# Kernel optimization log

Measured on AMD Instinct MI355X. Metric: run time of the kernel, lower is better.

The kernel has to match this reference:

```python
import jax, jax.numpy as jnp
import numpy as np
from jax import lax

B, G = 8, 64
V = G * G * G  # 262144, matches fc1 in-features


def setup_inputs() -> dict:
    key = jax.random.key(0)
    ks = jax.random.split(key, 10)
    boundary = (jax.random.uniform(ks[0], (B, 1, G, G, G)) < 0.1).astype(jnp.float32)
    conv1_w = jax.random.normal(ks[1], (64, 1, 3, 3, 3), jnp.float32) * 0.1
    conv1_b = jax.random.normal(ks[2], (64,), jnp.float32) * 0.01
    conv2_w = jax.random.normal(ks[3], (1, 64, 3, 3, 3), jnp.float32) * 0.05
    conv2_b = jax.random.normal(ks[4], (1,), jnp.float32) * 0.01
    fc1_w = jax.random.normal(ks[5], (256, V), jnp.float32) * (1.0 / np.sqrt(V))
    fc1_b = jax.random.normal(ks[6], (256,), jnp.float32) * 0.01
    fc2_w = jax.random.normal(ks[7], (1, 256), jnp.float32) * (1.0 / 16.0)
    fc2_b = jax.random.normal(ks[8], (1,), jnp.float32) * 0.01
    noise = jax.random.uniform(ks[9], (B, V), jnp.float32)
    return {"boundary": boundary, "conv1_w": conv1_w, "conv1_b": conv1_b,
            "conv2_w": conv2_w, "conv2_b": conv2_b, "fc1_w": fc1_w,
            "fc1_b": fc1_b, "fc2_w": fc2_w, "fc2_b": fc2_b,
            "noise": noise, "num_points": 10}


def _conv3d(x, w, b):
    # NCDHW / OIDHW, stride 1, padding 1 with k=3 -> SAME
    y = lax.conv_general_dilated(x, w, (1, 1, 1), 'SAME',
                                 dimension_numbers=('NCDHW', 'OIDHW', 'NCDHW'))
    return y + b[None, :, None, None, None]


def _generate_points(boundary, noise, num_points):
    # Vectorized equivalent of the per-point rejection loop:
    # uniform sampling without replacement over cells where boundary == 0.
    bflat = boundary.reshape(boundary.shape[0], -1)  # [B, V]
    scores = jnp.where(bflat > 0.5, -jnp.inf, noise)
    _, idx = lax.top_k(scores, num_points)  # [B, k]
    rows = jnp.arange(bflat.shape[0])[:, None]
    pts = jnp.zeros_like(bflat).at[rows, idx].set(1.0)
    return pts.reshape(boundary.shape)


def reference(boundary, conv1_w, conv1_b, conv2_w, conv2_b,
              fc1_w, fc1_b, fc2_w, fc2_b, noise, num_points):
    x = jax.nn.relu(_conv3d(boundary, conv1_w, conv1_b))
    x = jax.nn.relu(_conv3d(x, conv2_w, conv2_b))
    x = x.reshape(x.shape[0], -1)                      # [B, V]
    x = jax.nn.relu(x @ fc1_w.T + fc1_b)               # [B, 256]
    probability = jax.nn.sigmoid(x @ fc2_w.T + fc2_b) * 100.0  # [B, 1]
    points = _generate_points(boundary, noise, num_points)
    return points, probability
```

## Files before the change

### kernel.cpp

```cpp
#include <hip/hip_runtime.h>
#include <math.h>

#define G 64
#define GV (G*G*G)
#define NB 8
#define NP 9

typedef unsigned short u16;
typedef unsigned int u32;
typedef unsigned long long U64;
typedef __bf16 bf16x8 __attribute__((ext_vector_type(8)));
typedef float f32x4 __attribute__((ext_vector_type(4)));

union BF8 { u16 s[8]; bf16x8 v; };

__device__ __forceinline__ float bf2f(u16 h) {
    union { u32 u; float f; } c; c.u = ((u32)h) << 16; return c.f;
}
__device__ __forceinline__ u16 f2bf(float f) {
    union { float f; u32 u; } c; c.f = f;
    u32 u = c.u;
    return (u16)((u + 0x7fffu + ((u >> 16) & 1u)) >> 16);
}
__device__ __forceinline__ u32 cvt_pk_bf16(float lo, float hi) {
    u32 r;
    asm volatile("v_cvt_pk_bf16_f32 %0, %1, %2" : "=v"(r) : "v"(lo), "v"(hi));
    return r;
}

#define YSTRIDE 36

__global__ __launch_bounds__(256) void convA_mfma_kernel(
    const float* __restrict__ bnd,
    const float* __restrict__ w1, const float* __restrict__ b1,
    const float* __restrict__ w2,
    u16* __restrict__ zbuf)
{
    int b = blockIdx.y;
    const float* bd = bnd + (size_t)b * GV;
    u16* zb = zbuf + (size_t)b * (NP * (size_t)GV);

    __shared__ __align__(16) u16 halo[2378];
    __shared__ __align__(16) u32 Ylds[4][66 * YSTRIDE];

    int tid = threadIdx.x;
    int z0 = (blockIdx.x >> 4) * 4, y0 = (blockIdx.x & 15) * 4;

    {
        float* ldsW = (float*)&Ylds[0][0];
        for (int i = tid; i < 3520; i += 256) {
            float v;
            if (i < 1728)      v = w1[i];
            else if (i < 3456) v = w2[i - 1728];
            else               v = b1[i - 3456];
            ldsW[i] = v;
        }
    }

    for (int i = tid; i < 2378; i += 256) {
        u16 hval = 0;
        if (i < 2376) {
            int hz = i / 396, rem = i - hz * 396;
            int hy = rem / 66, hx = rem - hy * 66;
            int gz = z0 + hz - 1, gy = y0 + hy - 1, gx = hx - 1;
            if (((unsigned)gz < (unsigned)G) & ((unsigned)gy < (unsigned)G) &
                ((unsigned)gx < (unsigned)G)) {
                float f = bd[(gz << 12) + (gy << 6) + gx];
                hval = (f > 0.5f) ? (u16)0x3F80 : (u16)0;
            }
        }
        halo[i] = hval;
    }

    __syncthreads();

    int wv = tid >> 6, lane = tid & 63;
    int g = lane >> 4, lr = lane & 15;

    const float* ldsW = (const float*)&Ylds[0][0];
    BF8 w1A[4];
#pragma unroll
    for (int m = 0; m < 4; m++) {
        int c = 16 * m + lr;
#pragma unroll
        for (int j = 0; j < 8; j++) {
            int kk = 8 * g + j;
            float w = (kk < 27) ? ldsW[c * 27 + kk] : 0.0f;
            w1A[m].s[j] = f2bf(w);
        }
    }
    BF8 w2dx[3][2];
#pragma unroll
    for (int dx = 0; dx < 3; dx++)
#pragma unroll
        for (int ks = 0; ks < 2; ks++)
#pragma unroll
            for (int j = 0; j < 8; j++) {
                int ch = 32 * ks + 8 * g + j;
                float w = (lr < NP) ? ldsW[1728 + ch * 27 + 3 * lr + dx] : 0.0f;
                w2dx[dx][ks].s[j] = f2bf(w);
            }
    float bias[4][4];
#pragma unroll
    for (int m = 0; m < 4; m++)
#pragma unroll
        for (int r = 0; r < 4; r++) bias[m][r] = ldsW[3456 + 16 * m + 4 * g + r];

    int tapoff[8];
#pragma unroll
    for (int j = 0; j < 8; j++) {
        int kk = 8 * g + j;
        int kc = kk < 27 ? kk : 0;
        int dz = kc / 9, ry = kc - dz * 9;
        int dy = ry / 3, dxx = ry - dy * 3;
        tapoff[j] = dz * 396 + dy * 66 + dxx;
    }

    __syncthreads();

    u32* myY = &Ylds[wv][0];

    for (int li = 0; li < 4; li++) {
        int l = wv * 4 + li;
        int zl = l >> 2, yl = l & 3;
        int linebase = (zl * 6 + yl) * 66 + lr;
        int vbase = ((z0 + zl) << 12) + ((y0 + yl) << 6);

        myY[(lane < 32 ? 0 : 65 * YSTRIDE) + (lane & 31)] = 0;

        for (int xt = 0; xt < 4; xt++) {
            int x0 = xt * 16;
            BF8 xB;
#pragma unroll
            for (int j = 0; j < 8; j++)
                xB.s[j] = halo[linebase + x0 + tapoff[j]];

            f32x4 yac[4];
#pragma unroll
            for (int m = 0; m < 4; m++) {
                f32x4 c0;
                c0[0] = bias[m][0]; c0[1] = bias[m][1];
                c0[2] = bias[m][2]; c0[3] = bias[m][3];
                yac[m] = __builtin_amdgcn_mfma_f32_16x16x32_bf16(
                    w1A[m].v, xB.v, c0, 0, 0, 0);
            }

            int rx = x0 + lr + 1;
#pragma unroll
            for (int m = 0; m < 4; m++) {
                float a0 = fmaxf(yac[m][0], 0.f), a1 = fmaxf(yac[m][1], 0.f);
                float a2 = fmaxf(yac[m][2], 0.f), a3 = fmaxf(yac[m][3], 0.f);
                u32 h01 = cvt_pk_bf16(a0, a1);
                u32 h23 = cvt_pk_bf16(a2, a3);
                *(U64*)&myY[rx * YSTRIDE + 8 * m + 2 * g] =
                    (U64)h01 | ((U64)h23 << 32);
            }
        }

        asm volatile("" ::: "memory");

        for (int xt = 0; xt < 4; xt++) {
            int x0 = xt * 16;
            f32x4 zac = f32x4{0.f, 0.f, 0.f, 0.f};
#pragma unroll
            for (int dx = 0; dx < 3; dx++) {
                int rbase = (x0 + lr + dx) * YSTRIDE;
#pragma unroll
                for (int ks = 0; ks < 2; ks++) {
                    bf16x8 yB = *(const bf16x8*)&myY[rbase + 16 * ks + 4 * g];
                    zac = __builtin_amdgcn_mfma_f32_16x16x32_bf16(
                        w2dx[dx][ks].v, yB, zac, 0, 0, 0);
                }
            }

            int vg = vbase + x0 + lr;
#pragma unroll
            for (int r = 0; r < 4; r++) {
                int p = 4 * g + r;
                if (p < NP)
                    zb[(size_t)p * GV + vg] = f2bf(zac[r]);
            }
        }

        asm volatile("" ::: "memory");
    }
}

#define BPB 32
#define IDXM 0x3FFFFu

__global__ __launch_bounds__(256) void convB_topk_kernel(
    const u16* __restrict__ zbuf, float* __restrict__ xout,
    const float* __restrict__ b2,
    const float* __restrict__ bnd, const float* __restrict__ noise,
    U64* __restrict__ cand, float4* __restrict__ pts_out)
{
    __shared__ U64 lcand[256 * 10];
    __shared__ U64 rv[256];
    __shared__ int rp[256];

    int tid = threadIdx.x;

    if (blockIdx.x >= 256) {
        int r = blockIdx.x - 256;
        int vblk = r & 1023, b = r >> 10;
        const u16* zb = zbuf + (size_t)b * (NP * (size_t)GV);
        float* xo = xout + (size_t)b * GV;

        int v  = vblk * 256 + tid;
        int zc = v >> 12, yc = (v >> 6) & 63, xc = v & 63;
        float acc = b2[0];
#pragma unroll
        for (int dz = 0; dz < 3; dz++)
#pragma unroll
        for (int dy = 0; dy < 3; dy++) {
            int p = dz * 3 + dy;
            int zz = zc + dz - 1, yy = yc + dy - 1;
            bool ok = ((unsigned)zz < (unsigned)G) & ((unsigned)yy < (unsigned)G);
            if (ok) acc += bf2f(zb[(size_t)p * GV + (zz << 12) + (yy << 6) + xc]);
        }
        xo[v] = fmaxf(acc, 0.0f);
        return;
    }

    int blk = blockIdx.x & 31;
    int b   = blockIdx.x >> 5;
    int vbase = blk * (GV / BPB);

    float4* zp = pts_out + ((size_t)b * GV + vbase) / 4;
#pragma unroll
    for (int i = 0; i < 8; i++)
        zp[i * 256 + tid] = make_float4(0.f, 0.f, 0.f, 0.f);

    const float* bd = bnd + (size_t)b * GV + vbase;
    const float* nz = noise + (size_t)b * GV + vbase;

    U64 top[10];
#pragma unroll
    for (int k = 0; k < 10; k++) top[k] = 0ull;

    for (int i = 0; i < (GV / BPB) / 256; i++) {
        int e = i * 256 + tid;
        float bv = bd[e];
        float s  = nz[e];
        U64 p = (bv > 0.5f) ? 0ull
              : ((((U64)__float_as_uint(s)) << 32) |
                 (IDXM - (unsigned)(vbase + e)));
        if (p > top[9]) {
#pragma unroll
            for (int k = 0; k < 10; k++) {
                U64 mx = p > top[k] ? p : top[k];
                U64 mn = p > top[k] ? top[k] : p;
                top[k] = mx; p = mn;
            }
        }
    }

#pragma unroll
    for (int k = 0; k < 10; k++) lcand[tid * 10 + k] = top[k];
    __syncthreads();

    for (int pass = 0; pass < 10; pass++) {
        U64 bv = 0; int bp = 0;
        for (int i = tid; i < 2560; i += 256) {
            U64 xv = lcand[i];
            if (xv > bv) { bv = xv; bp = i; }
        }
        rv[tid] = bv; rp[tid] = bp;
        __syncthreads();
        for (int off = 128; off > 0; off >>= 1) {
            if (tid < off) {
                if (rv[tid + off] > rv[tid]) { rv[tid] = rv[tid + off]; rp[tid] = rp[tid + off]; }
            }
            __syncthreads();
        }
        if (tid == 0) {
            cand[((size_t)b * BPB + blk) * 10 + pass] = rv[0];
            lcand[rp[0]] = 0ull;
        }
        __syncthreads();
    }
}

__global__ __launch_bounds__(256) void fc1_kernel(
    const float* __restrict__ W, const float* __restrict__ x,
    float* __restrict__ pacc)
{
    int bid = blockIdx.x;
    int xcd  = bid & 7;
    int slot = bid >> 3;
    int vc = (xcd << 3) | (slot >> 5);
    int jt = slot & 31;
    int tid = threadIdx.x;
    int j0 = jt * 8;
    size_t v0 = (size_t)vc * 4096;

    const f32x4* Wp[8];
#pragma unroll
    for (int jj = 0; jj < 8; jj++)
        Wp[jj] = reinterpret_cast<const f32x4*>(W + (size_t)(j0 + jj) * GV + v0);
    const f32x4* Xp[NB];
#pragma unroll
    for (int b = 0; b < NB; b++)
        Xp[b] = reinterpret_cast<const f32x4*>(x + (size_t)b * GV + v0);

    float acc[8][NB];
#pragma unroll
    for (int jj = 0; jj < 8; jj++)
#pragma unroll
        for (int b = 0; b < NB; b++) acc[jj][b] = 0.0f;

    for (int i = 0; i < 4; i++) {
        int e = i * 256 + tid;
        f32x4 wvv[8];
#pragma unroll
        for (int jj = 0; jj < 8; jj++)
            wvv[jj] = __builtin_nontemporal_load(&Wp[jj][e]);
        f32x4 xv[NB];
#pragma unroll
        for (int b = 0; b < NB; b++) xv[b] = Xp[b][e];
#pragma unroll
        for (int b = 0; b < NB; b++) {
#pragma unroll
            for (int jj = 0; jj < 8; jj++) {
                acc[jj][b] = fmaf(wvv[jj][0], xv[b][0], acc[jj][b]);
                acc[jj][b] = fmaf(wvv[jj][1], xv[b][1], acc[jj][b]);
                acc[jj][b] = fmaf(wvv[jj][2], xv[b][2], acc[jj][b]);
                acc[jj][b] = fmaf(wvv[jj][3], xv[b][3], acc[jj][b]);
            }
        }
    }

    __shared__ float sacc[256][36];
    __shared__ float p2[8][40];
#pragma unroll
    for (int pass = 0; pass < 2; pass++) {
        if (pass > 0) __syncthreads();
        float4* row = reinterpret_cast<float4*>(&sacc[tid][0]);
#pragma unroll
        for (int jj = 0; jj < 4; jj++) {
            int js = pass * 4 + jj;
            row[jj * 2 + 0] = make_float4(acc[js][0], acc[js][1], acc[js][2], acc[js][3]);
            row[jj * 2 + 1] = make_float4(acc[js][4], acc[js][5], acc[js][6], acc[js][7]);
        }
        __syncthreads();
        {
            int o = tid & 31, gg = tid >> 5;
            float s = 0.0f;
#pragma unroll
            for (int k = 0; k < 32; k++) s += sacc[gg * 32 + k][o];
            p2[gg][o] = s;
        }
        __syncthreads();
        if (tid < 32) {
            float s = 0.0f;
#pragma unroll
            for (int gg = 0; gg < 8; gg++) s += p2[gg][tid];
            int jj = tid >> 3, b = tid & 7;
            pacc[((size_t)b * 64 + vc) * 256 + (j0 + pass * 4 + jj)] = s;
        }
    }
}

__global__ __launch_bounds__(256) void finalize_kernel(
    const U64* __restrict__ cand, float* __restrict__ pts,
    const float* __restrict__ pacc, const float* __restrict__ fc1_b,
    const float* __restrict__ fc2_w, const float* __restrict__ fc2_b,
    float* __restrict__ prob)
{
    int tid = threadIdx.x;

    if (blockIdx.x < 8) {
        int b = blockIdx.x;
        __shared__ U64 lc[BPB * 10];
        __shared__ U64 rv[256];
        __shared__ int rp[256];
        __shared__ int widx[10];
        for (int i = tid; i < BPB * 10; i += 256) lc[i] = cand[(size_t)b * BPB * 10 + i];
        __syncthreads();

        for (int pass = 0; pass < 10; pass++) {
            U64 bv = 0; int bp = 0;
            for (int i = tid; i < BPB * 10; i += 256) {
                U64 xv = lc[i];
                if (xv > bv) { bv = xv; bp = i; }
            }
            rv[tid] = bv; rp[tid] = bp;
            __syncthreads();
            for (int off = 128; off > 0; off >>= 1) {
                if (tid < off) {
                    if (rv[tid + off] > rv[tid]) { rv[tid] = rv[tid + off]; rp[tid] = rp[tid + off]; }
                }
                __syncthreads();
            }
            if (tid == 0) { widx[pass] = (int)(IDXM - (u32)(rv[0] & 0xffffffffu)); lc[rp[0]] = 0ull; }
            __syncthreads();
        }
        if (tid < 10) pts[(size_t)b * GV + widx[tid]] = 1.0f;
    } else {
        int j = tid;
        float h[NB];
#pragma unroll
        for (int b = 0; b < NB; b++) h[b] = 0.0f;
        for (int c = 0; c < 64; c++) {
#pragma unroll
            for (int b = 0; b < NB; b++)
                h[b] += pacc[((size_t)b * 64 + c) * 256 + j];
        }
        float w2j = fc2_w[j];
        float contrib[NB];
#pragma unroll
        for (int b = 0; b < NB; b++)
            contrib[b] = fmaxf(h[b] + fc1_b[j], 0.0f) * w2j;

        int lane = j & 63, wid = j >> 6;
#pragma unroll
        for (int b = 0; b < NB; b++)
#pragma unroll
            for (int off = 32; off > 0; off >>= 1)
                contrib[b] += __shfl_down(contrib[b], off, 64);

        __shared__ float sred[4][NB];
        if (lane == 0) {
#pragma unroll
            for (int b = 0; b < NB; b++) sred[wid][b] = contrib[b];
        }
        __syncthreads();
        if (j < NB) {
            float t = sred[0][j] + sred[1][j] + sred[2][j] + sred[3][j] + fc2_b[0];
            prob[j] = 100.0f / (1.0f + expf(-t));
        }
    }
}

extern "C" void kernel_launch(void* const* d_in, const int* in_sizes, int n_in,
                              void* d_out, int out_size, void* d_ws, size_t ws_size,
                              hipStream_t stream)
{
    const float* bnd   = (const float*)d_in[0];
    const float* w1    = (const float*)d_in[1];
    const float* b1    = (const float*)d_in[2];
    const float* w2    = (const float*)d_in[3];
    const float* b2    = (const float*)d_in[4];
    const float* fw1   = (const float*)d_in[5];
    const float* fb1   = (const float*)d_in[6];
    const float* fw2   = (const float*)d_in[7];
    const float* fb2   = (const float*)d_in[8];
    const float* noise = (const float*)d_in[9];

    float* out = (float*)d_out;
    char* ws = (char*)d_ws;

    const size_t xbuf_off = 0;
    const size_t pacc_off = xbuf_off + (size_t)NB * GV * 4;
    const size_t cand_off = pacc_off + (size_t)NB * 64 * 256 * 4;
    const size_t zbuf_off = cand_off + (size_t)NB * BPB * 10 * 8;

    float* xbuf = (float*)(ws + xbuf_off);
    float* pacc = (float*)(ws + pacc_off);
    U64*   cand = (U64*)(ws + cand_off);
    u16*   zbuf = (u16*)(ws + zbuf_off);

    dim3 gA(256, NB);
    convA_mfma_kernel<<<gA, 256, 0, stream>>>(bnd, w1, b1, w2, zbuf);

    convB_topk_kernel<<<8448, 256, 0, stream>>>(zbuf, xbuf, b2, bnd, noise,
                                                cand, (float4*)out);

    fc1_kernel<<<2048, 256, 0, stream>>>(fw1, xbuf, pacc);

    finalize_kernel<<<9, 256, 0, stream>>>(cand, out, pacc, fb1, fw2, fb2,
                                           out + (size_t)NB * GV);
}
```

Before: 172.2 us.

## Move top-k point sampling from convB launch into convA launch

The top-k candidate selection and point-zeroing blocks move out of the convB kernel and into the convA kernel as extra leading blocks. Their shared memory is overlaid with convA's halo and Y buffers in one pool. The aim is to run the memory-bound top-k work alongside the compute-bound MFMA conv, so the convB launch only does the cheap stencil sum. The cost is a larger shared-memory footprint per block, which may lower convA occupancy, and top-k blocks may finish unevenly relative to the conv blocks.

```diff
diff --git a/kernel.cpp b/kernel.cpp
--- a/kernel.cpp
+++ b/kernel.cpp
@@ -29,25 +29,97 @@
 }
 
 #define YSTRIDE 36
-
-__global__ __launch_bounds__(256) void convA_mfma_kernel(
+#define BPB 32
+#define IDXM 0x3FFFFu
+#define POOLB 42784
+
+__global__ __launch_bounds__(256) void convA_topk_kernel(
     const float* __restrict__ bnd,
     const float* __restrict__ w1, const float* __restrict__ b1,
     const float* __restrict__ w2,
-    u16* __restrict__ zbuf)
+    u16* __restrict__ zbuf,
+    const float* __restrict__ noise,
+    U64* __restrict__ cand, float4* __restrict__ pts_out)
 {
-    int b = blockIdx.y;
+    __shared__ __align__(16) char pool[POOLB];
+    int tid = threadIdx.x;
+
+    if (blockIdx.x < 256) {
+        int blk = blockIdx.x & 31;
+        int b   = blockIdx.x >> 5;
+        int vbase = blk * (GV / BPB);
+
+        float4* zp = pts_out + ((size_t)b * GV + vbase) / 4;
+#pragma unroll
+        for (int i = 0; i < 8; i++)
+            zp[i * 256 + tid] = make_float4(0.f, 0.f, 0.f, 0.f);
+
+        const float* bd = bnd + (size_t)b * GV + vbase;
+        const float* nz = noise + (size_t)b * GV + vbase;
+
+        U64 top[10];
+#pragma unroll
+        for (int k = 0; k < 10; k++) top[k] = 0ull;
+
+        for (int i = 0; i < (GV / BPB) / 256; i++) {
+            int e = i * 256 + tid;
+            float bv = bd[e];
+            float s  = nz[e];
+            U64 p = (bv > 0.5f) ? 0ull
+                  : ((((U64)__float_as_uint(s)) << 32) |
+                     (IDXM - (unsigned)(vbase + e)));
+            if (p > top[9]) {
+#pragma unroll
+                for (int k = 0; k < 10; k++) {
+                    U64 mx = p > top[k] ? p : top[k];
+                    U64 mn = p > top[k] ? top[k] : p;
+                    top[k] = mx; p = mn;
+                }
+            }
+        }
+
+        U64* lcand = (U64*)pool;
+        U64* rv    = (U64*)(pool + 20480);
+        int* rp    = (int*)(pool + 22528);
+#pragma unroll
+        for (int k = 0; k < 10; k++) lcand[tid * 10 + k] = top[k];
+        __syncthreads();
+
+        for (int pass = 0; pass < 10; pass++) {
+            U64 bv = 0; int bp = 0;
+            for (int i = tid; i < 2560; i += 256) {
+                U64 xv = lcand[i];
+                if (xv > bv) { bv = xv; bp = i; }
+            }
+            rv[tid] = bv; rp[tid] = bp;
+            __syncthreads();
+            for (int off = 128; off > 0; off >>= 1) {
+                if (tid < off) {
+                    if (rv[tid + off] > rv[tid]) { rv[tid] = rv[tid + off]; rp[tid] = rp[tid + off]; }
+                }
+                __syncthreads();
+            }
+            if (tid == 0) {
+                cand[((size_t)b * BPB + blk) * 10 + pass] = rv[0];
+                lcand[rp[0]] = 0ull;
+            }
+            __syncthreads();
+        }
+        return;
+    }
+
+    int bid = blockIdx.x - 256;
+    int box = bid & 255, b = bid >> 8;
     const float* bd = bnd + (size_t)b * GV;
     u16* zb = zbuf + (size_t)b * (NP * (size_t)GV);
 
-    __shared__ __align__(16) u16 halo[2378];
-    __shared__ __align__(16) u32 Ylds[4][66 * YSTRIDE];
-
-    int tid = threadIdx.x;
-    int z0 = (blockIdx.x >> 4) * 4, y0 = (blockIdx.x & 15) * 4;
+    u16* halo  = (u16*)pool;
+    u32* ybase = (u32*)(pool + 4768);
+
+    int z0 = (box >> 4) * 4, y0 = (box & 15) * 4;
 
     {
-        float* ldsW = (float*)&Ylds[0][0];
+        float* ldsW = (float*)ybase;
         for (int i = tid; i < 3520; i += 256) {
             float v;
             if (i < 1728)      v = w1[i];
@@ -77,7 +149,7 @@
     int wv = tid >> 6, lane = tid & 63;
     int g = lane >> 4, lr = lane & 15;
 
-    const float* ldsW = (const float*)&Ylds[0][0];
+    const float* ldsW = (const float*)ybase;
     BF8 w1A[4];
 #pragma unroll
     for (int m = 0; m < 4; m++) {
@@ -118,7 +190,7 @@
 
     __syncthreads();
 
-    u32* myY = &Ylds[wv][0];
+    u32* myY = ybase + wv * (66 * YSTRIDE);
 
     for (int li = 0; li < 4; li++) {
         int l = wv * 4 + li;
@@ -186,100 +258,28 @@
     }
 }
 
-#define BPB 32
-#define IDXM 0x3FFFFu
-
-__global__ __launch_bounds__(256) void convB_topk_kernel(
-    const u16* __restrict__ zbuf, float* __restrict__ xout,
-    const float* __restrict__ b2,
-    const float* __restrict__ bnd, const float* __restrict__ noise,
-    U64* __restrict__ cand, float4* __restrict__ pts_out)
+__global__ __launch_bounds__(256) void convB_kernel(
+    const u16* __restrict__ zbuf,
+    float* __restrict__ xout,
+    const float* __restrict__ b2)
 {
-    __shared__ U64 lcand[256 * 10];
-    __shared__ U64 rv[256];
-    __shared__ int rp[256];
-
-    int tid = threadIdx.x;
-
-    if (blockIdx.x >= 256) {
-        int r = blockIdx.x - 256;
-        int vblk = r & 1023, b = r >> 10;
-        const u16* zb = zbuf + (size_t)b * (NP * (size_t)GV);
-        float* xo = xout + (size_t)b * GV;
-
-        int v  = vblk * 256 + tid;
-        int zc = v >> 12, yc = (v >> 6) & 63, xc = v & 63;
-        float acc = b2[0];
-#pragma unroll
-        for (int dz = 0; dz < 3; dz++)
-#pragma unroll
-        for (int dy = 0; dy < 3; dy++) {
-            int p = dz * 3 + dy;
-            int zz = zc + dz - 1, yy = yc + dy - 1;
-            bool ok = ((unsigned)zz < (unsigned)G) & ((unsigned)yy < (unsigned)G);
-            if (ok) acc += bf2f(zb[(size_t)p * GV + (zz << 12) + (yy << 6) + xc]);
-        }
-        xo[v] = fmaxf(acc, 0.0f);
-        return;
-    }
-
-    int blk = blockIdx.x & 31;
-    int b   = blockIdx.x >> 5;
-    int vbase = blk * (GV / BPB);
-
-    float4* zp = pts_out + ((size_t)b * GV + vbase) / 4;
-#pragma unroll
-    for (int i = 0; i < 8; i++)
-        zp[i * 256 + tid] = make_float4(0.f, 0.f, 0.f, 0.f);
-
-    const float* bd = bnd + (size_t)b * GV + vbase;
-    const float* nz = noise + (size_t)b * GV + vbase;
-
-    U64 top[10];
-#pragma unroll
-    for (int k = 0; k < 10; k++) top[k] = 0ull;
-
-    for (int i = 0; i < (GV / BPB) / 256; i++) {
-        int e = i * 256 + tid;
-        float bv = bd[e];
-        float s  = nz[e];
-        U64 p = (bv > 0.5f) ? 0ull
-              : ((((U64)__float_as_uint(s)) << 32) |
-                 (IDXM - (unsigned)(vbase + e)));
-        if (p > top[9]) {
-#pragma unroll
-            for (int k = 0; k < 10; k++) {
-                U64 mx = p > top[k] ? p : top[k];
-                U64 mn = p > top[k] ? top[k] : p;
-                top[k] = mx; p = mn;
-            }
-        }
-    }
-
-#pragma unroll
-    for (int k = 0; k < 10; k++) lcand[tid * 10 + k] = top[k];
-    __syncthreads();
-
-    for (int pass = 0; pass < 10; pass++) {
-        U64 bv = 0; int bp = 0;
-        for (int i = tid; i < 2560; i += 256) {
-            U64 xv = lcand[i];
-            if (xv > bv) { bv = xv; bp = i; }
-        }
-        rv[tid] = bv; rp[tid] = bp;
-        __syncthreads();
-        for (int off = 128; off > 0; off >>= 1) {
-            if (tid < off) {
-                if (rv[tid + off] > rv[tid]) { rv[tid] = rv[tid + off]; rp[tid] = rp[tid + off]; }
-            }
-            __syncthreads();
-        }
-        if (tid == 0) {
-            cand[((size_t)b * BPB + blk) * 10 + pass] = rv[0];
-            lcand[rp[0]] = 0ull;
-        }
-        __syncthreads();
-    }
+    int b = blockIdx.y;
+    const u16* zb = zbuf + (size_t)b * (NP * (size_t)GV);
+    float* xo = xout + (size_t)b * GV;
+
+    int v  = blockIdx.x * 256 + threadIdx.x;
+    int zc = v >> 12, yc = (v >> 6) & 63, xc = v & 63;
+    float acc = b2[0];
+#pragma unroll
+    for (int dz = 0; dz < 3; dz++)
+#pragma unroll
+    for (int dy = 0; dy < 3; dy++) {
+        int p = dz * 3 + dy;
+        int zz = zc + dz - 1, yy = yc + dy - 1;
+        bool ok = ((unsigned)zz < (unsigned)G) & ((unsigned)yy < (unsigned)G);
+        if (ok) acc += bf2f(zb[(size_t)p * GV + (zz << 12) + (yy << 6) + xc]);
+    }
+    xo[v] = fmaxf(acc, 0.0f);
 }
 
 __global__ __launch_bounds__(256) void fc1_kernel(
@@ -461,11 +461,11 @@
     U64*   cand = (U64*)(ws + cand_off);
     u16*   zbuf = (u16*)(ws + zbuf_off);
 
-    dim3 gA(256, NB);
-    convA_mfma_kernel<<<gA, 256, 0, stream>>>(bnd, w1, b1, w2, zbuf);
-
-    convB_topk_kernel<<<8448, 256, 0, stream>>>(zbuf, xbuf, b2, bnd, noise,
-                                                cand, (float4*)out);
+    convA_topk_kernel<<<2304, 256, 0, stream>>>(bnd, w1, b1, w2, zbuf,
+                                                noise, cand, (float4*)out);
+
+    dim3 gB(GV / 256, NB);
+    convB_kernel<<<gB, 256, 0, stream>>>(zbuf, xbuf, b2);
 
     fc1_kernel<<<2048, 256, 0, stream>>>(fw1, xbuf, pacc);
 
```

After: 164.9 us. -4.2%, faster.
